# Kernel tuning notes

Hardware: AMD Instinct MI355X
Metric: run time of the kernel (lower is better)

The kernel has to match this reference:

```python
import jax, jax.numpy as jnp
import numpy as np

B, C, H, W = 16, 256, 64, 64


def _conv1x1(x, w, b):
    # x: [B,C,H,W], w: [O,C], b: [O]
    return jnp.einsum('oc,bchw->bohw', w, x) + b[None, :, None, None]


def _maxpool2(x):
    b, c, h, w = x.shape
    return x.reshape(b, c, h // 2, 2, w // 2, 2).max(axis=(3, 5))


def setup_inputs() -> dict:
    key = jax.random.key(0)
    ks = jax.random.split(key, 10)
    c8, c2 = C // 8, C // 2
    s = lambda fan_in: 1.0 / np.sqrt(fan_in)
    return {
        'x': jax.random.normal(ks[0], (B, C, H, W), dtype=jnp.float32),
        'query_w': jax.random.normal(ks[1], (c8, C), dtype=jnp.float32) * s(C),
        'query_b': jnp.zeros((c8,), dtype=jnp.float32),
        'key_w': jax.random.normal(ks[2], (c8, C), dtype=jnp.float32) * s(C),
        'key_b': jnp.zeros((c8,), dtype=jnp.float32),
        'val_w': jax.random.normal(ks[3], (c2, C), dtype=jnp.float32) * s(C),
        'val_b': jnp.zeros((c2,), dtype=jnp.float32),
        'val2_w': jax.random.normal(ks[4], (C, c2), dtype=jnp.float32) * s(c2),
        'val2_b': jnp.zeros((C,), dtype=jnp.float32),
        'gamma': jnp.zeros((1,), dtype=jnp.float32) + 0.5,  # nonzero so attention path contributes
    }


def reference(x, query_w, query_b, key_w, key_b, val_w, val_b, val2_w, val2_b, gamma):
    b, nc, h, w = x.shape
    loc = h * w
    down = loc // 4
    c8, c2 = nc // 8, nc // 2

    # query: conv then raw view to [B, HW, C//8] (NOT a permute; faithful to torch .view)
    q = _conv1x1(x, query_w, query_b)              # [B, C/8, H, W]
    q = q.reshape(b, loc, c8)                      # raw reshape, mixes channel/spatial

    # key: conv -> 2x2 maxpool -> raw view -> permute(0,2,1)
    k = _maxpool2(_conv1x1(x, key_w, key_b))       # [B, C/8, H/2, W/2]
    k = k.reshape(b, down, c8).transpose(0, 2, 1)  # [B, C/8, down]

    # value: conv -> 2x2 maxpool -> raw view
    v = _maxpool2(_conv1x1(x, val_w, val_b))       # [B, C/2, H/2, W/2]
    v = v.reshape(b, down, c2)                     # [B, down, C/2]

    attn = jnp.einsum('bqd,bdk->bqk', q, k)        # [B, HW, down], no 1/sqrt(d)
    attn_weights = jax.nn.softmax(attn, axis=1)    # softmax over QUERY axis (dim=1), as in source
    applied = jnp.einsum('bqk,bkc->bqc', attn_weights, v)  # [B, HW, C/2]

    # raw view back to [B, C/2, w, h] (note w,h swapped in source)
    applied = applied.reshape(b, c2, w, h)
    out = _conv1x1(applied, val2_w, val2_b)        # [B, C, w, h]
    return gamma * out + x
```

## Files before the change

### kernel.cpp

```cpp
#include <hip/hip_runtime.h>
#include <hip/hip_bf16.h>


typedef short s8v __attribute__((ext_vector_type(8)));
typedef float f4v __attribute__((ext_vector_type(4)));
typedef unsigned short u16v8 __attribute__((ext_vector_type(8)));

#define MFMA16(a, b, c) __builtin_amdgcn_mfma_f32_16x16x32_bf16((a), (b), (c), 0, 0, 0)
#define LOG2E 1.4426950408889634f

__device__ __forceinline__ unsigned short f2b(float f) {
    __hip_bfloat16 h = __float2bfloat16(f);
    return *reinterpret_cast<unsigned short*>(&h);
}
__device__ __forceinline__ float b2f(unsigned short u) {
    union { unsigned int i; float f; } v; v.i = ((unsigned int)u) << 16; return v.f;
}
__device__ __forceinline__ void async_lds16(const void* g, void* l) {
    __builtin_amdgcn_global_load_lds(
        (const __attribute__((address_space(1))) void*)g,
        (__attribute__((address_space(3))) void*)l, 16, 0, 0);
}

__global__ __launch_bounds__(256) void prologue(const float* __restrict__ x,
                                                unsigned short* __restrict__ xbt,
                                                const float* __restrict__ qw, const float* __restrict__ qb,
                                                const float* __restrict__ kw, const float* __restrict__ kb,
                                                const float* __restrict__ vw, const float* __restrict__ vb,
                                                const float* __restrict__ v2w,
                                                unsigned short* __restrict__ wqkv,
                                                float* __restrict__ bias,
                                                unsigned short* __restrict__ w2b) {
    int bid = blockIdx.x;
    if (bid < 4096) {
        __shared__ float tile[64][65];
        int bx = bid & 3, by = (bid >> 2) & 63, bz = bid >> 8;
        size_t base = (size_t)bz * 1048576;
        int r0 = bx * 64, c0 = by * 64;
        int rl = threadIdx.x >> 3;
        int g  = threadIdx.x & 7;
        #pragma unroll
        for (int rr = 0; rr < 2; ++rr) {
            int r = rr * 32 + rl;
            const float* p = x + base + (size_t)(r0 + r) * 4096 + c0 + g * 8;
            float4 a = *(const float4*)p;
            float4 bq = *(const float4*)(p + 4);
            tile[r][g * 8 + 0] = a.x;  tile[r][g * 8 + 1] = a.y;
            tile[r][g * 8 + 2] = a.z;  tile[r][g * 8 + 3] = a.w;
            tile[r][g * 8 + 4] = bq.x; tile[r][g * 8 + 5] = bq.y;
            tile[r][g * 8 + 6] = bq.z; tile[r][g * 8 + 7] = bq.w;
        }
        __syncthreads();
        #pragma unroll
        for (int rr = 0; rr < 2; ++rr) {
            int c = rr * 32 + rl;
            u16v8 o;
            #pragma unroll
            for (int i = 0; i < 8; ++i) o[i] = f2b(tile[g * 8 + i][c]);
            *(u16v8*)(xbt + base + (size_t)(c0 + c) * 256 + r0 + g * 8) = o;
        }
    } else {
        int i = (bid - 4096) * 256 + threadIdx.x;
        if (i < 49152) {
            int r = i >> 8, c = i & 255; float v;
            if (r < 32)       v = qw[r * 256 + c];
            else if (r < 64)  v = kw[(r - 32) * 256 + c] * LOG2E;
            else              v = vw[(r - 64) * 256 + c];
            wqkv[i] = f2b(v);
        } else if (i < 49152 + 32768) {
            int k = i - 49152; w2b[k] = f2b(v2w[k]);
        } else if (i < 49152 + 32768 + 192) {
            int r = i - 49152 - 32768;
            bias[r] = (r < 32) ? qb[r] : (r < 64 ? kb[r - 32] * LOG2E : vb[r - 64]);
        }
    }
}

__global__ __launch_bounds__(256) void transpose_scale_v(const unsigned short* __restrict__ src,
                                                         const float* __restrict__ rs,
                                                         unsigned short* __restrict__ dst) {
    __shared__ float tile[64][65];
    int b = blockIdx.z;
    size_t base = (size_t)b * 131072;
    int r0 = blockIdx.x * 64, c0 = blockIdx.y * 64;
    int tr = threadIdx.x >> 6, tc = threadIdx.x & 63;
    float scale = rs[b * 1024 + r0 + tc];
    for (int i = 0; i < 16; ++i) {
        int rl = i * 4 + tr;
        tile[rl][tc] = b2f(src[base + (size_t)(r0 + rl) * 128 + c0 + tc]);
    }
    __syncthreads();
    for (int i = 0; i < 16; ++i) {
        int cl = i * 4 + tr;
        int c = c0 + cl;
        int j = r0 + tc;
        int jc = j >> 7, jl = j & 127, g = jl >> 3, e = jl & 7;
        dst[base + jc * 16384 + c * 128 + ((g ^ (c & 7)) << 3) + e] =
            f2b(tile[tc][cl] * scale);
    }
}

__global__ __launch_bounds__(256) void qkv_pool(const unsigned short* __restrict__ wqkv,
                                                const float* __restrict__ bias,
                                                const unsigned short* __restrict__ xbt,
                                                unsigned short* __restrict__ qf,
                                                unsigned short* __restrict__ kf,
                                                unsigned short* __restrict__ vf) {
    int b = blockIdx.y, r = blockIdx.x;
    int p0 = r * 128;
    int wave = threadIdx.x >> 6, lane = threadIdx.x & 63;
    int m = lane & 15, quad = lane >> 4;
    const unsigned short* xb = xbt + (size_t)b * 4096 * 256;

    f4v acc[3][8] = {};
    for (int ks = 0; ks < 8; ++ks) {
        int k0 = ks * 32 + quad * 8;
        s8v afr[3];
        for (int mt = 0; mt < 3; ++mt)
            afr[mt] = *(const s8v*)(wqkv + (wave * 48 + mt * 16 + m) * 256 + k0);
        for (int nt = 0; nt < 8; ++nt) {
            s8v bfr = *(const s8v*)(xb + (size_t)(p0 + nt * 16 + m) * 256 + k0);
            for (int mt = 0; mt < 3; ++mt)
                acc[mt][nt] = MFMA16(afr[mt], bfr, acc[mt][nt]);
        }
    }
    for (int mt = 0; mt < 3; ++mt) {
        int obase = wave * 48 + mt * 16;
        if (obase < 32) {
            for (int reg = 0; reg < 4; ++reg) {
                int o = obase + quad * 4 + reg;
                float bi = bias[o];
                for (int nt = 0; nt < 8; ++nt)
                    qf[(size_t)b * 131072 + (size_t)o * 4096 + p0 + nt * 16 + m] =
                        f2b(acc[mt][nt][reg] + bi);
            }
        } else {
            for (int reg = 0; reg < 4; ++reg) {
                int o = obase + quad * 4 + reg;
                float bi = bias[o];
                for (int nt = 0; nt < 4; ++nt) {
                    float vv = fmaxf(acc[mt][nt][reg], acc[mt][nt + 4][reg]);
                    float ov = __shfl_xor(vv, 1);
                    if ((m & 1) == 0) {
                        float res = fmaxf(vv, ov) + bi;
                        int w2 = nt * 8 + (m >> 1);
                        int sp = r * 32 + w2;
                        if (o < 64) kf[(size_t)b * 32768 + (size_t)(o - 32) * 1024 + sp] = f2b(res);
                        else        vf[(size_t)b * 131072 + (size_t)(o - 64) * 1024 + sp] = f2b(res);
                    }
                }
            }
        }
    }
}

__global__ __launch_bounds__(256) void col_stats(const unsigned short* __restrict__ qf,
                                                 const unsigned short* __restrict__ kf,
                                                 float* __restrict__ rs) {
    __shared__ float red[4][16];
    int b = blockIdx.y, j0 = blockIdx.x * 16;
    int wave = threadIdx.x >> 6, lane = threadIdx.x & 63;
    int m = lane & 15, quad = lane >> 4;
    const unsigned short* qb = qf + (size_t)b * 131072;
    f4v zero = {0.f, 0.f, 0.f, 0.f};

    s8v kfr = *(const s8v*)(kf + (size_t)b * 32768 + (size_t)(j0 + m) * 32 + quad * 8);

    float sm = 0.f;
    for (int it = wave; it < 256; it += 4) {
        s8v afr = *(const s8v*)(qb + (size_t)(it * 16 + m) * 32 + quad * 8);
        f4v s = MFMA16(afr, kfr, zero);
        sm += (exp2f(s[0]) + exp2f(s[1])) + (exp2f(s[2]) + exp2f(s[3]));
    }
    sm += __shfl_xor(sm, 16);
    sm += __shfl_xor(sm, 32);
    if (lane < 16) red[wave][m] = sm;
    __syncthreads();
    if (threadIdx.x < 16) {
        float S = (red[0][threadIdx.x] + red[1][threadIdx.x]) +
                  (red[2][threadIdx.x] + red[3][threadIdx.x]);
        rs[b * 1024 + j0 + threadIdx.x] = 1.0f / S;
    }
}

__global__ __launch_bounds__(256, 3) void attn_fused(const unsigned short* __restrict__ qf,
                                                     const unsigned short* __restrict__ kf,
                                                     const unsigned short* __restrict__ vsw,
                                                     unsigned short* __restrict__ fa) {
    __shared__ alignas(16) unsigned short VS[16384];
    __shared__ alignas(16) unsigned short PT[8192];
    int b = blockIdx.y, l0 = blockIdx.x * 64;
    int tid = threadIdx.x;
    int wave = tid >> 6, lane = tid & 63;
    int m = lane & 15, quad = lane >> 4;
    int ls = wave * 16;
    const unsigned short* qb = qf + (size_t)b * 131072;
    const unsigned short* kb = kf + (size_t)b * 32768;
    const unsigned short* vb = vsw + (size_t)b * 131072;

    s8v qa = *(const s8v*)(qb + (size_t)(l0 + ls + m) * 32 + quad * 8);
    f4v acc[8] = {};
    f4v zero = {0.f, 0.f, 0.f, 0.f};

    for (int jc = 0; jc < 8; ++jc) {
        {
            const unsigned short* src = vb + jc * 16384 + tid * 8;
            unsigned short* dstl = VS + tid * 8;
            for (int rnd = 0; rnd < 8; ++rnd)
                async_lds16(src + rnd * 2048, dstl + rnd * 2048);
        }
        int j0 = jc * 128;
        int l = ls + m;
        for (int jt = 0; jt < 8; ++jt) {
            s8v kfr = *(const s8v*)(kb + (size_t)(j0 + jt * 16 + m) * 32 + quad * 8);
            f4v st = MFMA16(kfr, qa, zero);
            unsigned int u0 = ((unsigned)f2b(exp2f(st[1])) << 16) |
                              (unsigned)f2b(exp2f(st[0]));
            unsigned int u1 = ((unsigned)f2b(exp2f(st[3])) << 16) |
                              (unsigned)f2b(exp2f(st[2]));
            int g = jt * 2 + (quad >> 1);
            int sub = (quad & 1) * 4;
            uint2 uu; uu.x = u0; uu.y = u1;
            *(uint2*)(&PT[l * 128 + ((g ^ (l & 7)) << 3) + sub]) = uu;
        }
        __syncthreads();
        __builtin_amdgcn_s_setprio(1);
        for (int ks = 0; ks < 4; ++ks) {
            int gp = ks * 4 + quad;
            s8v pa = *(const s8v*)(&PT[l * 128 + ((gp ^ (l & 7)) << 3)]);
            for (int ct = 0; ct < 8; ++ct) {
                int c = ct * 16 + m;
                s8v vfr = *(const s8v*)(&VS[c * 128 + ((gp ^ (c & 7)) << 3)]);
                acc[ct] = MFMA16(pa, vfr, acc[ct]);
            }
        }
        __builtin_amdgcn_s_setprio(0);
        __syncthreads();
    }
    for (int ct = 0; ct < 8; ++ct)
        for (int reg = 0; reg < 4; ++reg) {
            int l = l0 + ls + quad * 4 + reg;
            fa[(size_t)b * 524288 + (size_t)l * 128 + ct * 16 + m] = f2b(acc[ct][reg]);
        }
}

__global__ __launch_bounds__(256, 4) void final_gemm(const unsigned short* __restrict__ w2b,
                                                     const float* __restrict__ v2b,
                                                     const float* __restrict__ gamma,
                                                     const unsigned short* __restrict__ fa,
                                                     const float* __restrict__ x,
                                                     float* __restrict__ out) {
    __shared__ alignas(16) unsigned short gt[64][136];
    int b = blockIdx.z, bx = blockIdx.x;
    int p0 = bx * 64;
    int page = bx >> 1;
    int c0 = (bx & 1) * 64;
    int wave = threadIdx.x >> 6, lane = threadIdx.x & 63;
    int m = lane & 15, quad = lane >> 4;
    int obase = blockIdx.y * 128 + wave * 32;

    int row  = threadIdx.x >> 1;
    int half = threadIdx.x & 1;
    const unsigned short* fr = fa + (size_t)b * 524288 +
                               (size_t)(row * 32 + page) * 128 + c0 + half * 32;
    u16v8 t0 = *(const u16v8*)(fr);
    u16v8 t1 = *(const u16v8*)(fr + 8);
    u16v8 t2 = *(const u16v8*)(fr + 16);
    u16v8 t3 = *(const u16v8*)(fr + 24);

    float4 xv[2][4];
    #pragma unroll
    for (int mt = 0; mt < 2; ++mt) {
        size_t xrow = (size_t)b * 1048576 + (size_t)(obase + mt * 16 + m) * 4096;
        #pragma unroll
        for (int nt = 0; nt < 4; ++nt)
            xv[mt][nt] = *(const float4*)(x + xrow + p0 + nt * 16 + quad * 4);
    }

    {
        int pb = half * 32;
        #pragma unroll
        for (int i = 0; i < 8; ++i) {
            gt[pb + i][row]      = t0[i];
            gt[pb + 8 + i][row]  = t1[i];
            gt[pb + 16 + i][row] = t2[i];
            gt[pb + 24 + i][row] = t3[i];
        }
    }
    __syncthreads();

    f4v acc[2][4] = {};
    for (int ks = 0; ks < 4; ++ks) {
        int k0 = ks * 32 + quad * 8;
        s8v afr[2], bfr[4];
        #pragma unroll
        for (int mt = 0; mt < 2; ++mt)
            afr[mt] = *(const s8v*)(w2b + (obase + mt * 16 + m) * 128 + k0);
        #pragma unroll
        for (int nt = 0; nt < 4; ++nt)
            bfr[nt] = *(const s8v*)(&gt[nt * 16 + m][k0]);
        #pragma unroll
        for (int mt = 0; mt < 2; ++mt)
            #pragma unroll
            for (int nt = 0; nt < 4; ++nt)
                acc[mt][nt] = MFMA16(bfr[nt], afr[mt], acc[mt][nt]);
    }
    float g = gamma[0];
    #pragma unroll
    for (int mt = 0; mt < 2; ++mt) {
        int o = obase + mt * 16 + m;
        float bi = v2b[o];
        size_t xrow = (size_t)b * 1048576 + (size_t)o * 4096;
        #pragma unroll
        for (int nt = 0; nt < 4; ++nt) {
            size_t xi = xrow + p0 + nt * 16 + quad * 4;
            float4 ov;
            ov.x = g * (acc[mt][nt][0] + bi) + xv[mt][nt].x;
            ov.y = g * (acc[mt][nt][1] + bi) + xv[mt][nt].y;
            ov.z = g * (acc[mt][nt][2] + bi) + xv[mt][nt].z;
            ov.w = g * (acc[mt][nt][3] + bi) + xv[mt][nt].w;
            *(float4*)(out + xi) = ov;
        }
    }
}

extern "C" void kernel_launch(void* const* d_in, const int* in_sizes, int n_in,
                              void* d_out, int out_size, void* d_ws, size_t ws_size,
                              hipStream_t stream) {
    const float* x    = (const float*)d_in[0];
    const float* qw   = (const float*)d_in[1];
    const float* qb   = (const float*)d_in[2];
    const float* kw   = (const float*)d_in[3];
    const float* kb   = (const float*)d_in[4];
    const float* vw   = (const float*)d_in[5];
    const float* vb   = (const float*)d_in[6];
    const float* v2w  = (const float*)d_in[7];
    const float* v2b  = (const float*)d_in[8];
    const float* gamma = (const float*)d_in[9];
    float* out = (float*)d_out;

    char* ws = (char*)d_ws;
    size_t off = 0;
    auto alloc = [&](size_t bytes) { size_t o = off; off = (off + bytes + 255) & ~(size_t)255; return o; };
    unsigned short* wqkv = (unsigned short*)(ws + alloc(192 * 256 * 2));
    unsigned short* w2b  = (unsigned short*)(ws + alloc(256 * 128 * 2));
    float*          bias = (float*)(ws + alloc(192 * 4));
    float*          rs   = (float*)(ws + alloc((size_t)16 * 1024 * 4));
    unsigned short* qf   = (unsigned short*)(ws + alloc((size_t)16 * 131072 * 2));
    unsigned short* kf   = (unsigned short*)(ws + alloc((size_t)16 * 32768 * 2));
    unsigned short* vf   = (unsigned short*)(ws + alloc((size_t)16 * 131072 * 2));
    unsigned short* vt   = (unsigned short*)(ws + alloc((size_t)16 * 131072 * 2));
    unsigned short* fa   = (unsigned short*)(ws + alloc((size_t)16 * 524288 * 2));
    unsigned short* xbt  = (unsigned short*)(ws + alloc((size_t)16 * 4096 * 256 * 2));
    (void)ws_size; (void)in_sizes; (void)n_in; (void)out_size;

    prologue<<<4417, 256, 0, stream>>>(x, xbt, qw, qb, kw, kb, vw, vb, v2w, wqkv, bias, w2b);
    qkv_pool<<<dim3(32, 16), 256, 0, stream>>>(wqkv, bias, xbt, qf, kf, vf);
    col_stats<<<dim3(64, 16), 256, 0, stream>>>(qf, kf, rs);
    transpose_scale_v<<<dim3(16, 2, 16), 256, 0, stream>>>(vf, rs, vt);
    attn_fused<<<dim3(64, 16), 256, 0, stream>>>(qf, kf, vt, fa);
    final_gemm<<<dim3(64, 2, 16), 256, 0, stream>>>(w2b, v2b, gamma, fa, x, out);
}
```

Before: 259.9 us.

## Read V fragments directly from global and drop LDS staging and barriers

```diff
diff --git a/kernel.cpp b/kernel.cpp
--- a/kernel.cpp
+++ b/kernel.cpp
@@ -15,11 +15,6 @@
 }
 __device__ __forceinline__ float b2f(unsigned short u) {
     union { unsigned int i; float f; } v; v.i = ((unsigned int)u) << 16; return v.f;
-}
-__device__ __forceinline__ void async_lds16(const void* g, void* l) {
-    __builtin_amdgcn_global_load_lds(
-        (const __attribute__((address_space(1))) void*)g,
-        (__attribute__((address_space(3))) void*)l, 16, 0, 0);
 }
 
 __global__ __launch_bounds__(256) void prologue(const float* __restrict__ x,
@@ -92,11 +87,7 @@
     __syncthreads();
     for (int i = 0; i < 16; ++i) {
         int cl = i * 4 + tr;
-        int c = c0 + cl;
-        int j = r0 + tc;
-        int jc = j >> 7, jl = j & 127, g = jl >> 3, e = jl & 7;
-        dst[base + jc * 16384 + c * 128 + ((g ^ (c & 7)) << 3) + e] =
-            f2b(tile[tc][cl] * scale);
+        dst[base + (size_t)(c0 + cl) * 1024 + r0 + tc] = f2b(tile[tc][cl] * scale);
     }
 }
 
@@ -183,34 +174,27 @@
     }
 }
 
-__global__ __launch_bounds__(256, 3) void attn_fused(const unsigned short* __restrict__ qf,
+__global__ __launch_bounds__(512, 4) void attn_fused(const unsigned short* __restrict__ qf,
                                                      const unsigned short* __restrict__ kf,
-                                                     const unsigned short* __restrict__ vsw,
+                                                     const unsigned short* __restrict__ vtp,
                                                      unsigned short* __restrict__ fa) {
-    __shared__ alignas(16) unsigned short VS[16384];
-    __shared__ alignas(16) unsigned short PT[8192];
-    int b = blockIdx.y, l0 = blockIdx.x * 64;
+    __shared__ alignas(16) unsigned short PT[16384];
+    int b = blockIdx.y, l0 = blockIdx.x * 128;
     int tid = threadIdx.x;
     int wave = tid >> 6, lane = tid & 63;
     int m = lane & 15, quad = lane >> 4;
     int ls = wave * 16;
     const unsigned short* qb = qf + (size_t)b * 131072;
     const unsigned short* kb = kf + (size_t)b * 32768;
-    const unsigned short* vb = vsw + (size_t)b * 131072;
+    const unsigned short* vb = vtp + (size_t)b * 131072;
 
     s8v qa = *(const s8v*)(qb + (size_t)(l0 + ls + m) * 32 + quad * 8);
     f4v acc[8] = {};
     f4v zero = {0.f, 0.f, 0.f, 0.f};
+    int l = ls + m;
 
     for (int jc = 0; jc < 8; ++jc) {
-        {
-            const unsigned short* src = vb + jc * 16384 + tid * 8;
-            unsigned short* dstl = VS + tid * 8;
-            for (int rnd = 0; rnd < 8; ++rnd)
-                async_lds16(src + rnd * 2048, dstl + rnd * 2048);
-        }
         int j0 = jc * 128;
-        int l = ls + m;
         for (int jt = 0; jt < 8; ++jt) {
             s8v kfr = *(const s8v*)(kb + (size_t)(j0 + jt * 16 + m) * 32 + quad * 8);
             f4v st = MFMA16(kfr, qa, zero);
@@ -223,24 +207,22 @@
             uint2 uu; uu.x = u0; uu.y = u1;
             *(uint2*)(&PT[l * 128 + ((g ^ (l & 7)) << 3) + sub]) = uu;
         }
-        __syncthreads();
         __builtin_amdgcn_s_setprio(1);
         for (int ks = 0; ks < 4; ++ks) {
             int gp = ks * 4 + quad;
             s8v pa = *(const s8v*)(&PT[l * 128 + ((gp ^ (l & 7)) << 3)]);
             for (int ct = 0; ct < 8; ++ct) {
                 int c = ct * 16 + m;
-                s8v vfr = *(const s8v*)(&VS[c * 128 + ((gp ^ (c & 7)) << 3)]);
+                s8v vfr = *(const s8v*)(vb + (size_t)c * 1024 + j0 + gp * 8);
                 acc[ct] = MFMA16(pa, vfr, acc[ct]);
             }
         }
         __builtin_amdgcn_s_setprio(0);
-        __syncthreads();
     }
     for (int ct = 0; ct < 8; ++ct)
         for (int reg = 0; reg < 4; ++reg) {
-            int l = l0 + ls + quad * 4 + reg;
-            fa[(size_t)b * 524288 + (size_t)l * 128 + ct * 16 + m] = f2b(acc[ct][reg]);
+            int lo = l0 + ls + quad * 4 + reg;
+            fa[(size_t)b * 524288 + (size_t)lo * 128 + ct * 16 + m] = f2b(acc[ct][reg]);
         }
 }
 
@@ -358,6 +340,6 @@
     qkv_pool<<<dim3(32, 16), 256, 0, stream>>>(wqkv, bias, xbt, qf, kf, vf);
     col_stats<<<dim3(64, 16), 256, 0, stream>>>(qf, kf, rs);
     transpose_scale_v<<<dim3(16, 2, 16), 256, 0, stream>>>(vf, rs, vt);
-    attn_fused<<<dim3(64, 16), 256, 0, stream>>>(qf, kf, vt, fa);
+    attn_fused<<<dim3(32, 16), 512, 0, stream>>>(qf, kf, vt, fa);
     final_gemm<<<dim3(64, 2, 16), 256, 0, stream>>>(w2b, v2b, gamma, fa, x, out);
 }
```

After: 343.8 us. 1.32x slower.
